# Kernel optimization log

Measured on AMD Instinct MI355X. Metric: run time of the kernel, lower is better.

## Reference

```python
import jax, jax.numpy as jnp
import numpy as np

NUM_HEADS = 16
HEAD_DIM = 64  # embedding_dim 1024 / 16


def setup_inputs() -> dict:
    key = jax.random.key(0)
    k1, k2, k3, k4 = jax.random.split(key, 4)
    B, S, D = 2, 2048, 1024
    return {
        "query": jax.random.normal(k1, (B, S, D), dtype=jnp.float32),
        "key": jax.random.normal(k2, (B, S, D), dtype=jnp.float32),
        "value": jax.random.normal(k3, (B, S, D), dtype=jnp.float32),
        "W_out": jax.random.normal(k4, (D, D), dtype=jnp.float32) * (1.0 / np.sqrt(D)),
        "b_out": jnp.zeros((D,), dtype=jnp.float32),
    }


def reference(query, key, value, W_out, b_out):
    B, S, D = query.shape
    H, hd = NUM_HEADS, HEAD_DIM
    # NOTE: original forward never applies q_fc/k_fc/v_fc (transform ignores fc)
    q = query.reshape(B, S, H, hd).transpose(0, 2, 1, 3)  # [B,H,S,hd]
    k = key.reshape(B, S, H, hd).transpose(0, 2, 1, 3)
    v = value.reshape(B, S, H, hd).transpose(0, 2, 1, 3)
    scores = jnp.einsum("bhqd,bhkd->bhqk", q, k) / jnp.sqrt(jnp.float32(hd))
    probs = jax.nn.softmax(scores, axis=-1)  # mask=None, dropout=None
    ctx = jnp.einsum("bhqk,bhkd->bhqd", probs, v)
    ctx = ctx.transpose(0, 2, 1, 3).reshape(B, S, D)
    return ctx @ W_out.T + b_out
```

## Files before the change

kernel.cpp:

```cpp
#include <hip/hip_runtime.h>
#include <hip/hip_bf16.h>
#include <stdint.h>

#define NB 2
#define SEQ 2048
#define DIM 1024
#define NH 16
#define HD 64

typedef __attribute__((ext_vector_type(4))) float f32x4;
typedef __attribute__((ext_vector_type(16))) float f32x16;
typedef __attribute__((ext_vector_type(8))) short s16x8;
typedef __attribute__((ext_vector_type(4))) short s16x4;
typedef __attribute__((ext_vector_type(8))) __bf16 bf16x8;

static __device__ __forceinline__ short f2bf_rne(float x) {
  uint32_t u = __float_as_uint(x);
  u += 0x7fffu + ((u >> 16) & 1u);
  return (short)(u >> 16);
}
static __device__ __forceinline__ uint32_t pk_bf16(float a, float b) {
  __hip_bfloat162 h = __float22bfloat162_rn(float2{a, b});
  uint32_t u;
  __builtin_memcpy(&u, &h, 4);
  return u;
}
static __device__ __forceinline__ bf16x8 ldfrag(const short* p) {
  bf16x8 r;
  __builtin_memcpy(&r, p, 16);
  return r;
}
static __device__ __forceinline__ void glds16(const short* g, short* l) {
  __builtin_amdgcn_global_load_lds(
      (const __attribute__((address_space(1))) uint32_t*)g,
      (__attribute__((address_space(3))) uint32_t*)l, 16, 0, 0);
}

__global__ __launch_bounds__(256) void prep_all(const float* __restrict__ K,
                                                const float* __restrict__ V,
                                                const float* __restrict__ W,
                                                short* __restrict__ Kh,
                                                short* __restrict__ Vt,
                                                short* __restrict__ Wh) {
  __shared__ float vtile[64][65];
  const int tid = threadIdx.x;
  const int id = blockIdx.x;

  if (id >= 1024) {
    size_t idx = ((size_t)(id - 1024) * 256 + tid) * 8;
    f32x4 a = *(const f32x4*)(W + idx);
    f32x4 b = *(const f32x4*)(W + idx + 4);
    s16x8 o;
#pragma unroll
    for (int j = 0; j < 4; ++j) {
      o[j] = f2bf_rne(a[j]);
      o[4 + j] = f2bf_rne(b[j]);
    }
    *(s16x8*)(Wh + idx) = o;
    return;
  }

  const int t0 = (id & 31) * 64;
  const int bh = id >> 5;
  const int b = bh >> 4, h = bh & 15;

#pragma unroll
  for (int i = 0; i < 4; ++i) {
    int f = tid + 256 * i;
    int row = f >> 4;
    int col = (f & 15) * 4;
    const float* src = K + ((size_t)(b * SEQ + t0 + row)) * DIM + h * HD + col;
    f32x4 v = *(const f32x4*)src;
    s16x4 hi;
#pragma unroll
    for (int j = 0; j < 4; ++j) hi[j] = f2bf_rne(v[j]);
    int kvh = row >> 5, l32r = row & 31;
    int ks = col >> 4, hl2 = (col >> 3) & 1, j0 = col & 7;
    *(s16x4*)(Kh + ((size_t)(bh * SEQ + t0)) * HD + kvh * 2048 + ks * 512 +
              l32r * 16 + hl2 * 8 + j0) = hi;
  }
#pragma unroll
  for (int i = 0; i < 4; ++i) {
    int f = tid + 256 * i;
    int row = f >> 4;
    int col = (f & 15) * 4;
    const float* src = V + ((size_t)(b * SEQ + t0 + row)) * DIM + h * HD + col;
    f32x4 v = *(const f32x4*)src;
#pragma unroll
    for (int j = 0; j < 4; ++j) vtile[row][col + j] = v[j];
  }
  __syncthreads();
#pragma unroll
  for (int i = 0; i < 4; ++i) {
    int idx = tid + 256 * i;
    int d = idx >> 4;
    int kb = (idx & 15) * 4;
    int kp = (kb & ~12) | ((kb & 4) << 1) | ((kb & 8) >> 1);
    s16x4 o4;
#pragma unroll
    for (int j = 0; j < 4; ++j) o4[j] = f2bf_rne(vtile[kb + j][d]);
    *(s16x4*)(Vt + ((size_t)bh * HD + d) * SEQ + t0 + kp) = o4;
  }
}

#define QSCALE (0.125f * 1.44269504088896340736f)
#define NT_KV 32

static __device__ __forceinline__ void exppv32(const f32x16& sf, const short* vb,
                                               int kvh, int l32, int hl,
                                               f32x16* acc, float& den0,
                                               float& den1) {
#pragma unroll
  for (int tp = 0; tp < 2; ++tp) {
    uint32_t w[4];
#pragma unroll
    for (int j2 = 0; j2 < 4; ++j2) {
      float p0 = __builtin_amdgcn_exp2f(sf[tp * 8 + j2 * 2]);
      float p1 = __builtin_amdgcn_exp2f(sf[tp * 8 + j2 * 2 + 1]);
      den0 += p0;
      den1 += p1;
      w[j2] = pk_bf16(p0, p1);
    }
    bf16x8 pa;
    __builtin_memcpy(&pa, w, 16);
    const int ksg = kvh * 2 + tp;
#pragma unroll
    for (int dt = 0; dt < 2; ++dt) {
      bf16x8 vf = ldfrag(vb + (dt * 32 + l32) * 64 +
                         (((ksg * 2 + hl) ^ (l32 & 7)) * 8));
      acc[dt] =
          __builtin_amdgcn_mfma_f32_32x32x16_bf16(pa, vf, acc[dt], 0, 0, 0);
    }
  }
}

static __device__ __forceinline__ f32x16 qkreg(const bf16x8* kf,
                                               const bf16x8* qh) {
  f32x16 s;
#pragma unroll
  for (int r = 0; r < 16; ++r) s[r] = 0.f;
#pragma unroll
  for (int ks = 0; ks < 4; ++ks)
    s = __builtin_amdgcn_mfma_f32_32x32x16_bf16(kf[ks], qh[ks], s, 0, 0, 0);
  return s;
}

__global__ __launch_bounds__(512, 4) void attn(const float* __restrict__ Q,
                                               const short* __restrict__ Kh,
                                               const short* __restrict__ Vt,
                                               short* __restrict__ Ch) {
  __shared__ __align__(16) short vbuf[2][4096];
  __shared__ __align__(16) float xbuf[4096];
  __shared__ float dsh[8][64];

  const int tid = threadIdx.x;
  const int wv = tid >> 6, ln = tid & 63;
  const int l32 = ln & 31, hl = ln >> 5;
  const int qsub = wv >> 1, kvh = wv & 1;
  const int bh = blockIdx.y, b = bh >> 4, hh = bh & 15;
  const int q0 = blockIdx.x * 128 + qsub * 32;

  bf16x8 qh[4];
  {
    const float* qp = Q + ((size_t)(b * SEQ + q0 + l32)) * DIM + hh * HD + hl * 8;
#pragma unroll
    for (int ks = 0; ks < 4; ++ks) {
      short th[8];
#pragma unroll
      for (int j = 0; j < 8; ++j) th[j] = f2bf_rne(qp[ks * 16 + j] * QSCALE);
      __builtin_memcpy(&qh[ks], th, 16);
    }
  }

  f32x16 acc[2];
#pragma unroll
  for (int r = 0; r < 16; ++r) {
    acc[0][r] = 0.f;
    acc[1][r] = 0.f;
  }
  float den0 = 0.f, den1 = 0.f;

  const short* khg =
      Kh + (size_t)bh * SEQ * HD + kvh * 2048 + l32 * 16 + hl * 8;
  const short* vtg = Vt + (size_t)bh * HD * SEQ;

  const int srow8 = ln >> 3;
  const int sg = ln & 7;
  const int sw = (sg ^ srow8) * 8;
  const int srow = wv * 8 + srow8;

  bf16x8 kf0[4];
#pragma unroll
  for (int ks = 0; ks < 4; ++ks) kf0[ks] = ldfrag(khg + ks * 512);
  glds16(vtg + (size_t)srow * SEQ + sw, &vbuf[0][wv * 512]);
  f32x16 sfA = qkreg(kf0, qh);

  for (int t = 0; t < 30; t += 2) {
    __syncthreads();
    bf16x8 kfa[4];
#pragma unroll
    for (int ks = 0; ks < 4; ++ks)
      kfa[ks] = ldfrag(khg + (t + 1) * 4096 + ks * 512);
    glds16(vtg + (size_t)srow * SEQ + (t + 1) * 64 + sw, &vbuf[1][wv * 512]);
    exppv32(sfA, &vbuf[0][0], kvh, l32, hl, acc, den0, den1);
    f32x16 sfB = qkreg(kfa, qh);
    __syncthreads();
    bf16x8 kfb[4];
#pragma unroll
    for (int ks = 0; ks < 4; ++ks)
      kfb[ks] = ldfrag(khg + (t + 2) * 4096 + ks * 512);
    glds16(vtg + (size_t)srow * SEQ + (t + 2) * 64 + sw, &vbuf[0][wv * 512]);
    exppv32(sfB, &vbuf[1][0], kvh, l32, hl, acc, den0, den1);
    sfA = qkreg(kfb, qh);
  }
  __syncthreads();
  bf16x8 kfl[4];
#pragma unroll
  for (int ks = 0; ks < 4; ++ks) kfl[ks] = ldfrag(khg + 31 * 4096 + ks * 512);
  glds16(vtg + (size_t)srow * SEQ + 31 * 64 + sw, &vbuf[1][wv * 512]);
  exppv32(sfA, &vbuf[0][0], kvh, l32, hl, acc, den0, den1);
  f32x16 sfT = qkreg(kfl, qh);
  __syncthreads();
  exppv32(sfT, &vbuf[1][0], kvh, l32, hl, acc, den0, den1);

  float den = den0 + den1;
  den += __shfl_xor(den, 32);

  f32x16 give, keep;
  if (kvh == 0) {
    give = acc[1];
    keep = acc[0];
  } else {
    give = acc[0];
    keep = acc[1];
  }

  __syncthreads();
  float* xr = (wv < 4) ? &xbuf[0] : (float*)&vbuf[0][0];
  *(f32x16*)(xr + (wv & 3) * 1024 + ln * 16) = give;
  dsh[wv][ln] = den;
  __syncthreads();

  float dtot = den + dsh[wv ^ 1][ln];
  float invd = 1.0f / dtot;
  float inv_r[16];
#pragma unroll
  for (int r = 0; r < 16; ++r)
    inv_r[r] = __shfl(invd, (r & 3) + 8 * (r >> 2) + 4 * hl, 64);

  f32x16 oth = *(const f32x16*)(xr + ((wv ^ 1) & 3) * 1024 + ln * 16);
#pragma unroll
  for (int r = 0; r < 16; ++r) {
    float cs = keep[r] + oth[r];
    int row = (r & 3) + 8 * (r >> 2) + 4 * hl;
    size_t off =
        ((size_t)(b * SEQ + q0 + row)) * DIM + hh * HD + kvh * 32 + l32;
    Ch[off] = f2bf_rne(cs * inv_r[r]);
  }
}

__global__ __launch_bounds__(512, 4) void proj(const short* __restrict__ Ah,
                                               const short* __restrict__ Wh,
                                               const float* __restrict__ bias,
                                               float* __restrict__ OUT) {
  __shared__ __align__(16) short ash[2][8192];
  __shared__ __align__(16) short wsh[2][8192];
  const int tid = threadIdx.x;
  const int wv = tid >> 6, ln = tid & 63;
  const int l32 = ln & 31, hl = ln >> 5;
  const int wm = wv >> 1, wn = wv & 1;
  const int m0 = blockIdx.x * 128, n0 = blockIdx.y * 128;

  f32x16 acc0, acc1;
#pragma unroll
  for (int r = 0; r < 16; ++r) {
    acc0[r] = 0.f;
    acc1[r] = 0.f;
  }

  const int srow8 = ln >> 3, sg = ln & 7;
  const int sw = (sg ^ srow8) * 8;

#pragma unroll
  for (int i = 0; i < 4; ++i) {
    int c = wv * 4 + i;
    int r8 = (c & 15) * 8 + srow8;
    if (c < 16)
      glds16(Ah + (size_t)(m0 + r8) * DIM + sw, ash[0] + (c & 15) * 512);
    else
      glds16(Wh + (size_t)(n0 + r8) * DIM + sw, wsh[0] + (c & 15) * 512);
  }

  for (int kt = 0; kt < DIM / 64; ++kt) {
    __syncthreads();
    if (kt + 1 < DIM / 64) {
      const int kk = (kt + 1) * 64;
      const int bn = (kt + 1) & 1;
#pragma unroll
      for (int i = 0; i < 4; ++i) {
        int c = wv * 4 + i;
        int r8 = (c & 15) * 8 + srow8;
        if (c < 16)
          glds16(Ah + (size_t)(m0 + r8) * DIM + kk + sw, ash[bn] + (c & 15) * 512);
        else
          glds16(Wh + (size_t)(n0 + r8) * DIM + kk + sw, wsh[bn] + (c & 15) * 512);
      }
    }
    const short* ab = ash[kt & 1];
    const short* wb = wsh[kt & 1];
#pragma unroll
    for (int ks = 0; ks < 4; ++ks) {
      int swz = ((ks * 2 + hl) ^ (l32 & 7)) * 8;
      bf16x8 af = ldfrag(ab + (wm * 32 + l32) * 64 + swz);
      bf16x8 wf0 = ldfrag(wb + (wn * 64 + l32) * 64 + swz);
      bf16x8 wf1 = ldfrag(wb + (wn * 64 + 32 + l32) * 64 + swz);
      acc0 = __builtin_amdgcn_mfma_f32_32x32x16_bf16(af, wf0, acc0, 0, 0, 0);
      acc1 = __builtin_amdgcn_mfma_f32_32x32x16_bf16(af, wf1, acc1, 0, 0, 0);
    }
  }

  float bs0 = bias[n0 + wn * 64 + l32];
  float bs1 = bias[n0 + wn * 64 + 32 + l32];
#pragma unroll
  for (int r = 0; r < 16; ++r) {
    int row = m0 + wm * 32 + (r & 3) + 8 * (r >> 2) + 4 * hl;
    int col = n0 + wn * 64 + l32;
    OUT[(size_t)row * DIM + col] = acc0[r] + bs0;
    OUT[(size_t)row * DIM + col + 32] = acc1[r] + bs1;
  }
}

extern "C" void kernel_launch(void* const* d_in, const int* in_sizes, int n_in,
                              void* d_out, int out_size, void* d_ws, size_t ws_size,
                              hipStream_t stream) {
  const float* Q = (const float*)d_in[0];
  const float* K = (const float*)d_in[1];
  const float* V = (const float*)d_in[2];
  const float* W = (const float*)d_in[3];
  const float* bias = (const float*)d_in[4];
  float* OUT = (float*)d_out;

  char* ws = (char*)d_ws;
  short* Kh = (short*)(ws + ((size_t)0 << 20));
  short* Vt = (short*)(ws + ((size_t)8 << 20));
  short* Ch = (short*)(ws + ((size_t)16 << 20));
  short* Wh = (short*)(ws + ((size_t)24 << 20));

  prep_all<<<dim3(1536), 256, 0, stream>>>(K, V, W, Kh, Vt, Wh);
  attn<<<dim3(SEQ / 128, NB * NH), 512, 0, stream>>>(Q, Kh, Vt, Ch);
  proj<<<dim3((NB * SEQ) / 128, DIM / 128), 512, 0, stream>>>(Ch, Wh, bias, OUT);
}
```

Before: 156.3 us.

## Halve attention block size and remap blocks so heads stay on one XCD

```diff
diff --git a/kernel.cpp b/kernel.cpp
--- a/kernel.cpp
+++ b/kernel.cpp
@@ -145,20 +145,25 @@
   return s;
 }
 
-__global__ __launch_bounds__(512, 4) void attn(const float* __restrict__ Q,
+__global__ __launch_bounds__(256, 4) void attn(const float* __restrict__ Q,
                                                const short* __restrict__ Kh,
                                                const short* __restrict__ Vt,
                                                short* __restrict__ Ch) {
   __shared__ __align__(16) short vbuf[2][4096];
-  __shared__ __align__(16) float xbuf[4096];
-  __shared__ float dsh[8][64];
+  __shared__ __align__(16) float xbuf[2048];
+  __shared__ float dsh[4][64];
 
   const int tid = threadIdx.x;
   const int wv = tid >> 6, ln = tid & 63;
   const int l32 = ln & 31, hl = ln >> 5;
   const int qsub = wv >> 1, kvh = wv & 1;
-  const int bh = blockIdx.y, b = bh >> 4, hh = bh & 15;
-  const int q0 = blockIdx.x * 128 + qsub * 32;
+
+  const int n = blockIdx.x;
+  const int xcd = n & 7, slot = n >> 3;
+  const int bh = xcd * 4 + (slot & 3);
+  const int bx = slot >> 2;
+  const int b = bh >> 4, hh = bh & 15;
+  const int q0 = bx * 64 + qsub * 32;
 
   bf16x8 qh[4];
   {
@@ -187,12 +192,16 @@
   const int srow8 = ln >> 3;
   const int sg = ln & 7;
   const int sw = (sg ^ srow8) * 8;
-  const int srow = wv * 8 + srow8;
 
   bf16x8 kf0[4];
 #pragma unroll
   for (int ks = 0; ks < 4; ++ks) kf0[ks] = ldfrag(khg + ks * 512);
-  glds16(vtg + (size_t)srow * SEQ + sw, &vbuf[0][wv * 512]);
+#pragma unroll
+  for (int i = 0; i < 2; ++i) {
+    int lc = wv * 2 + i;
+    int row = lc * 8 + srow8;
+    glds16(vtg + (size_t)row * SEQ + sw, &vbuf[0][lc * 512]);
+  }
   f32x16 sfA = qkreg(kf0, qh);
 
   for (int t = 0; t < 30; t += 2) {
@@ -201,7 +210,12 @@
 #pragma unroll
     for (int ks = 0; ks < 4; ++ks)
       kfa[ks] = ldfrag(khg + (t + 1) * 4096 + ks * 512);
-    glds16(vtg + (size_t)srow * SEQ + (t + 1) * 64 + sw, &vbuf[1][wv * 512]);
+#pragma unroll
+    for (int i = 0; i < 2; ++i) {
+      int lc = wv * 2 + i;
+      int row = lc * 8 + srow8;
+      glds16(vtg + (size_t)row * SEQ + (t + 1) * 64 + sw, &vbuf[1][lc * 512]);
+    }
     exppv32(sfA, &vbuf[0][0], kvh, l32, hl, acc, den0, den1);
     f32x16 sfB = qkreg(kfa, qh);
     __syncthreads();
@@ -209,7 +223,12 @@
 #pragma unroll
     for (int ks = 0; ks < 4; ++ks)
       kfb[ks] = ldfrag(khg + (t + 2) * 4096 + ks * 512);
-    glds16(vtg + (size_t)srow * SEQ + (t + 2) * 64 + sw, &vbuf[0][wv * 512]);
+#pragma unroll
+    for (int i = 0; i < 2; ++i) {
+      int lc = wv * 2 + i;
+      int row = lc * 8 + srow8;
+      glds16(vtg + (size_t)row * SEQ + (t + 2) * 64 + sw, &vbuf[0][lc * 512]);
+    }
     exppv32(sfB, &vbuf[1][0], kvh, l32, hl, acc, den0, den1);
     sfA = qkreg(kfb, qh);
   }
@@ -217,7 +236,12 @@
   bf16x8 kfl[4];
 #pragma unroll
   for (int ks = 0; ks < 4; ++ks) kfl[ks] = ldfrag(khg + 31 * 4096 + ks * 512);
-  glds16(vtg + (size_t)srow * SEQ + 31 * 64 + sw, &vbuf[1][wv * 512]);
+#pragma unroll
+  for (int i = 0; i < 2; ++i) {
+    int lc = wv * 2 + i;
+    int row = lc * 8 + srow8;
+    glds16(vtg + (size_t)row * SEQ + 31 * 64 + sw, &vbuf[1][lc * 512]);
+  }
   exppv32(sfA, &vbuf[0][0], kvh, l32, hl, acc, den0, den1);
   f32x16 sfT = qkreg(kfl, qh);
   __syncthreads();
@@ -236,8 +260,8 @@
   }
 
   __syncthreads();
-  float* xr = (wv < 4) ? &xbuf[0] : (float*)&vbuf[0][0];
-  *(f32x16*)(xr + (wv & 3) * 1024 + ln * 16) = give;
+  float* xr = (wv < 2) ? &xbuf[0] : (float*)&vbuf[0][0];
+  *(f32x16*)(xr + (wv & 1) * 1024 + ln * 16) = give;
   dsh[wv][ln] = den;
   __syncthreads();
 
@@ -248,7 +272,7 @@
   for (int r = 0; r < 16; ++r)
     inv_r[r] = __shfl(invd, (r & 3) + 8 * (r >> 2) + 4 * hl, 64);
 
-  f32x16 oth = *(const f32x16*)(xr + ((wv ^ 1) & 3) * 1024 + ln * 16);
+  f32x16 oth = *(const f32x16*)(xr + ((wv ^ 1) & 1) * 1024 + ln * 16);
 #pragma unroll
   for (int r = 0; r < 16; ++r) {
     float cs = keep[r] + oth[r];
@@ -347,6 +371,6 @@
   short* Wh = (short*)(ws + ((size_t)24 << 20));
 
   prep_all<<<dim3(1536), 256, 0, stream>>>(K, V, W, Kh, Vt, Wh);
-  attn<<<dim3(SEQ / 128, NB * NH), 512, 0, stream>>>(Q, Kh, Vt, Ch);
+  attn<<<dim3(1024), 256, 0, stream>>>(Q, Kh, Vt, Ch);
   proj<<<dim3((NB * SEQ) / 128, DIM / 128), 512, 0, stream>>>(Ch, Wh, bias, OUT);
 }
```

Measured after the change: 161.9 us. 1.04x slower.

## Load V fragments directly from global in MFMA layout, drop LDS staging

Applied to the files above, without the earlier changes.

```diff
diff --git a/kernel.cpp b/kernel.cpp
--- a/kernel.cpp
+++ b/kernel.cpp
@@ -99,17 +99,34 @@
     s16x4 o4;
 #pragma unroll
     for (int j = 0; j < 4; ++j) o4[j] = f2bf_rne(vtile[kb + j][d]);
-    *(s16x4*)(Vt + ((size_t)bh * HD + d) * SEQ + t0 + kp) = o4;
+    int dt = d >> 5, l32r = d & 31;
+    int ksg = kp >> 4, hl2 = (kp >> 3) & 1, j0 = kp & 7;
+    *(s16x4*)(Vt + ((size_t)(bh * 32 + (t0 >> 6))) * 4096 +
+              (ksg * 2 + dt) * 512 + l32r * 16 + hl2 * 8 + j0) = o4;
   }
 }
 
 #define QSCALE (0.125f * 1.44269504088896340736f)
-#define NT_KV 32
-
-static __device__ __forceinline__ void exppv32(const f32x16& sf, const short* vb,
-                                               int kvh, int l32, int hl,
-                                               f32x16* acc, float& den0,
-                                               float& den1) {
+
+static __device__ __forceinline__ f32x16 qkreg(const bf16x8& k0, const bf16x8& k1,
+                                               const bf16x8& k2, const bf16x8& k3,
+                                               const bf16x8* qh) {
+  f32x16 s;
+#pragma unroll
+  for (int r = 0; r < 16; ++r) s[r] = 0.f;
+  __builtin_amdgcn_s_setprio(1);
+  s = __builtin_amdgcn_mfma_f32_32x32x16_bf16(k0, qh[0], s, 0, 0, 0);
+  s = __builtin_amdgcn_mfma_f32_32x32x16_bf16(k1, qh[1], s, 0, 0, 0);
+  s = __builtin_amdgcn_mfma_f32_32x32x16_bf16(k2, qh[2], s, 0, 0, 0);
+  s = __builtin_amdgcn_mfma_f32_32x32x16_bf16(k3, qh[3], s, 0, 0, 0);
+  __builtin_amdgcn_s_setprio(0);
+  return s;
+}
+
+static __device__ __forceinline__ void exppv_reg(const f32x16& sf, bf16x8 v0,
+                                                 bf16x8 v1, bf16x8 v2,
+                                                 bf16x8 v3, f32x16* acc,
+                                                 float& den0, float& den1) {
 #pragma unroll
   for (int tp = 0; tp < 2; ++tp) {
     uint32_t w[4];
@@ -123,42 +140,31 @@
     }
     bf16x8 pa;
     __builtin_memcpy(&pa, w, 16);
-    const int ksg = kvh * 2 + tp;
-#pragma unroll
-    for (int dt = 0; dt < 2; ++dt) {
-      bf16x8 vf = ldfrag(vb + (dt * 32 + l32) * 64 +
-                         (((ksg * 2 + hl) ^ (l32 & 7)) * 8));
-      acc[dt] =
-          __builtin_amdgcn_mfma_f32_32x32x16_bf16(pa, vf, acc[dt], 0, 0, 0);
-    }
-  }
-}
-
-static __device__ __forceinline__ f32x16 qkreg(const bf16x8* kf,
-                                               const bf16x8* qh) {
-  f32x16 s;
-#pragma unroll
-  for (int r = 0; r < 16; ++r) s[r] = 0.f;
-#pragma unroll
-  for (int ks = 0; ks < 4; ++ks)
-    s = __builtin_amdgcn_mfma_f32_32x32x16_bf16(kf[ks], qh[ks], s, 0, 0, 0);
-  return s;
-}
-
-__global__ __launch_bounds__(512, 4) void attn(const float* __restrict__ Q,
+    acc[0] = __builtin_amdgcn_mfma_f32_32x32x16_bf16(pa, tp ? v2 : v0, acc[0],
+                                                     0, 0, 0);
+    acc[1] = __builtin_amdgcn_mfma_f32_32x32x16_bf16(pa, tp ? v3 : v1, acc[1],
+                                                     0, 0, 0);
+  }
+}
+
+__global__ __launch_bounds__(256, 3) void attn(const float* __restrict__ Q,
                                                const short* __restrict__ Kh,
                                                const short* __restrict__ Vt,
                                                short* __restrict__ Ch) {
-  __shared__ __align__(16) short vbuf[2][4096];
   __shared__ __align__(16) float xbuf[4096];
-  __shared__ float dsh[8][64];
+  __shared__ float dsh[4][64];
 
   const int tid = threadIdx.x;
   const int wv = tid >> 6, ln = tid & 63;
   const int l32 = ln & 31, hl = ln >> 5;
   const int qsub = wv >> 1, kvh = wv & 1;
-  const int bh = blockIdx.y, b = bh >> 4, hh = bh & 15;
-  const int q0 = blockIdx.x * 128 + qsub * 32;
+
+  const int n = blockIdx.x;
+  const int xcd = n & 7, slot = n >> 3;
+  const int bh = xcd * 4 + (slot & 3);
+  const int bx = slot >> 2;
+  const int b = bh >> 4, hh = bh & 15;
+  const int q0 = bx * 64 + qsub * 32;
 
   bf16x8 qh[4];
   {
@@ -180,48 +186,60 @@
   }
   float den0 = 0.f, den1 = 0.f;
 
-  const short* khg =
+  const short* kbase =
       Kh + (size_t)bh * SEQ * HD + kvh * 2048 + l32 * 16 + hl * 8;
-  const short* vtg = Vt + (size_t)bh * HD * SEQ;
-
-  const int srow8 = ln >> 3;
-  const int sg = ln & 7;
-  const int sw = (sg ^ srow8) * 8;
-  const int srow = wv * 8 + srow8;
-
-  bf16x8 kf0[4];
-#pragma unroll
-  for (int ks = 0; ks < 4; ++ks) kf0[ks] = ldfrag(khg + ks * 512);
-  glds16(vtg + (size_t)srow * SEQ + sw, &vbuf[0][wv * 512]);
-  f32x16 sfA = qkreg(kf0, qh);
-
+  const short* vbase =
+      Vt + (size_t)bh * (SEQ / 64) * 4096 + kvh * 2048 + l32 * 16 + hl * 8;
+
+  bf16x8 kA0 = ldfrag(kbase), kA1 = ldfrag(kbase + 512),
+         kA2 = ldfrag(kbase + 1024), kA3 = ldfrag(kbase + 1536);
+  bf16x8 vA0 = ldfrag(vbase), vA1 = ldfrag(vbase + 512),
+         vA2 = ldfrag(vbase + 1024), vA3 = ldfrag(vbase + 1536);
+  bf16x8 kB0 = ldfrag(kbase + 4096), kB1 = ldfrag(kbase + 4096 + 512),
+         kB2 = ldfrag(kbase + 4096 + 1024), kB3 = ldfrag(kbase + 4096 + 1536);
+  f32x16 sfA = qkreg(kA0, kA1, kA2, kA3, qh);
+
+  bf16x8 vB0, vB1, vB2, vB3;
   for (int t = 0; t < 30; t += 2) {
-    __syncthreads();
-    bf16x8 kfa[4];
-#pragma unroll
-    for (int ks = 0; ks < 4; ++ks)
-      kfa[ks] = ldfrag(khg + (t + 1) * 4096 + ks * 512);
-    glds16(vtg + (size_t)srow * SEQ + (t + 1) * 64 + sw, &vbuf[1][wv * 512]);
-    exppv32(sfA, &vbuf[0][0], kvh, l32, hl, acc, den0, den1);
-    f32x16 sfB = qkreg(kfa, qh);
-    __syncthreads();
-    bf16x8 kfb[4];
-#pragma unroll
-    for (int ks = 0; ks < 4; ++ks)
-      kfb[ks] = ldfrag(khg + (t + 2) * 4096 + ks * 512);
-    glds16(vtg + (size_t)srow * SEQ + (t + 2) * 64 + sw, &vbuf[0][wv * 512]);
-    exppv32(sfB, &vbuf[1][0], kvh, l32, hl, acc, den0, den1);
-    sfA = qkreg(kfb, qh);
-  }
-  __syncthreads();
-  bf16x8 kfl[4];
-#pragma unroll
-  for (int ks = 0; ks < 4; ++ks) kfl[ks] = ldfrag(khg + 31 * 4096 + ks * 512);
-  glds16(vtg + (size_t)srow * SEQ + 31 * 64 + sw, &vbuf[1][wv * 512]);
-  exppv32(sfA, &vbuf[0][0], kvh, l32, hl, acc, den0, den1);
-  f32x16 sfT = qkreg(kfl, qh);
-  __syncthreads();
-  exppv32(sfT, &vbuf[1][0], kvh, l32, hl, acc, den0, den1);
+    {
+      const short* kp2 = kbase + (size_t)(t + 2) * 4096;
+      kA0 = ldfrag(kp2);
+      kA1 = ldfrag(kp2 + 512);
+      kA2 = ldfrag(kp2 + 1024);
+      kA3 = ldfrag(kp2 + 1536);
+      const short* vp1 = vbase + (size_t)(t + 1) * 4096;
+      vB0 = ldfrag(vp1);
+      vB1 = ldfrag(vp1 + 512);
+      vB2 = ldfrag(vp1 + 1024);
+      vB3 = ldfrag(vp1 + 1536);
+    }
+    f32x16 sfB = qkreg(kB0, kB1, kB2, kB3, qh);
+    exppv_reg(sfA, vA0, vA1, vA2, vA3, acc, den0, den1);
+    {
+      const short* kp3 = kbase + (size_t)(t + 3) * 4096;
+      kB0 = ldfrag(kp3);
+      kB1 = ldfrag(kp3 + 512);
+      kB2 = ldfrag(kp3 + 1024);
+      kB3 = ldfrag(kp3 + 1536);
+      const short* vp2 = vbase + (size_t)(t + 2) * 4096;
+      vA0 = ldfrag(vp2);
+      vA1 = ldfrag(vp2 + 512);
+      vA2 = ldfrag(vp2 + 1024);
+      vA3 = ldfrag(vp2 + 1536);
+    }
+    sfA = qkreg(kA0, kA1, kA2, kA3, qh);
+    exppv_reg(sfB, vB0, vB1, vB2, vB3, acc, den0, den1);
+  }
+  {
+    const short* vp31 = vbase + (size_t)31 * 4096;
+    vB0 = ldfrag(vp31);
+    vB1 = ldfrag(vp31 + 512);
+    vB2 = ldfrag(vp31 + 1024);
+    vB3 = ldfrag(vp31 + 1536);
+  }
+  f32x16 sfT = qkreg(kB0, kB1, kB2, kB3, qh);
+  exppv_reg(sfA, vA0, vA1, vA2, vA3, acc, den0, den1);
+  exppv_reg(sfT, vB0, vB1, vB2, vB3, acc, den0, den1);
 
   float den = den0 + den1;
   den += __shfl_xor(den, 32);
@@ -235,9 +253,7 @@
     keep = acc[1];
   }
 
-  __syncthreads();
-  float* xr = (wv < 4) ? &xbuf[0] : (float*)&vbuf[0][0];
-  *(f32x16*)(xr + (wv & 3) * 1024 + ln * 16) = give;
+  *(f32x16*)(&xbuf[wv * 1024 + ln * 16]) = give;
   dsh[wv][ln] = den;
   __syncthreads();
 
@@ -248,7 +264,7 @@
   for (int r = 0; r < 16; ++r)
     inv_r[r] = __shfl(invd, (r & 3) + 8 * (r >> 2) + 4 * hl, 64);
 
-  f32x16 oth = *(const f32x16*)(xr + ((wv ^ 1) & 3) * 1024 + ln * 16);
+  f32x16 oth = *(const f32x16*)(&xbuf[(wv ^ 1) * 1024 + ln * 16]);
 #pragma unroll
   for (int r = 0; r < 16; ++r) {
     float cs = keep[r] + oth[r];
@@ -347,6 +363,6 @@
   short* Wh = (short*)(ws + ((size_t)24 << 20));
 
   prep_all<<<dim3(1536), 256, 0, stream>>>(K, V, W, Kh, Vt, Wh);
-  attn<<<dim3(SEQ / 128, NB * NH), 512, 0, stream>>>(Q, Kh, Vt, Ch);
+  attn<<<dim3(1024), 256, 0, stream>>>(Q, Kh, Vt, Ch);
   proj<<<dim3((NB * SEQ) / 128, DIM / 128), 512, 0, stream>>>(Ch, Wh, bias, OUT);
 }
```

Measured after the change: 176.4 us. +12.8%, slower.
